# Optimization experiments

Hardware: AMD Instinct MI355X
Metric: run time of the kernel (lower is better)

Reference implementation:

```python
import jax, jax.numpy as jnp
import numpy as np

CROP = 3          # crop_size
MAX_CROP = 2 * CROP  # 6 -> 6x6 = 36 offsets (faithful to range(max_crop))
H = 384


def reference(predict, target, target_mask):
    # mask both images
    t = target * target_mask
    p = predict * target_mask

    B, C, _, _ = p.shape
    hw = H - MAX_CROP  # 378

    # cropped target: [:, :, 3:-3, 3:-3] -> [B, C, 378, 378]
    ct = t[:, :, CROP:-CROP, CROP:-CROP]

    def c_mse_at(u, v):
        # shifted predict window [B, C, 378, 378]
        cp = jax.lax.dynamic_slice(p, (0, 0, u, v), (B, C, hw, hw))
        bb = jnp.mean(ct - cp)           # brightness bias (scalar)
        return jnp.mean((cp + bb - ct) ** 2)  # MSE after bias correction

    offs = jnp.arange(MAX_CROP)
    uu, vv = jnp.meshgrid(offs, offs, indexing='ij')
    losses = jax.vmap(c_mse_at)(uu.ravel(), vv.ravel())  # [36]

    cMSE = jnp.min(losses)
    score = -10.0 * jnp.log10(cMSE)  # cPSNR
    return score


def setup_inputs() -> dict:
    key = jax.random.key(0)
    k1, k2, k3 = jax.random.split(key, 3)
    shape = (32, 1, 384, 384)
    predict = jax.random.uniform(k1, shape, dtype=jnp.float32)
    target = jax.random.uniform(k2, shape, dtype=jnp.float32)
    target_mask = jax.random.uniform(k3, shape, dtype=jnp.float32)
    return {"predict": predict, "target": target, "target_mask": target_mask}
```

## Files before the change

kernel.cpp:

```cpp
#include <hip/hip_runtime.h>
#include <hip/hip_bf16.h>
#include <math.h>


#define NIMG 32
#define IMGSZ (384 * 384)
#define NRT 126
#define NSG 24
#define BSZ 128
#define NCC 756
#define NEDGE 64
#define CCPAD 760
#define CHUNK 95
#define NM 40
#define MSTRIDE 756
#define MQUADS 189
#define NE 262

__global__ __launch_bounds__(BSZ) void probav_fused_kernel(
    const float* __restrict__ predict,
    const float* __restrict__ target,
    const float* __restrict__ mask,
    float* __restrict__ mpart ,
    double* __restrict__ epart ) {

  const int t = threadIdx.x;
  const int lane = t & 63;
  const int w = t >> 6;

  if (blockIdx.x >= NEDGE) {
    const int i = blockIdx.x - NEDGE;
    const int cb = (i & 7) * CHUNK + (i >> 3);
    if (cb >= NCC) return;

    __shared__ float red[2 * NM];

    const int tid = cb * BSZ + t;
    const int img = tid / (NRT * NSG);
    const int rem = tid - img * (NRT * NSG);
    const int rt  = rem / NSG;
    const int sg  = rem - rt * NSG;
    const int r0  = rt * 3;
    const int jb  = sg * 16;
    const size_t base = (size_t)img * IMGSZ;
    const bool isLastRt = (rt == NRT - 1);

    int qc[6];
#pragma unroll
    for (int q = 0; q < 6; ++q) {
      int c = jb + 4 * q;
      qc[q] = (c > 380) ? 380 : c;
    }

    float ct[3][16];
    float t1 = 0.f, t2 = 0.f;
#pragma unroll
    for (int rr = 0; rr < 3; ++rr) {
      const float* trow = target + base + (size_t)(r0 + rr + 3) * 384;
      const float* mrow = mask   + base + (size_t)(r0 + rr + 3) * 384;
      float tv[20], mv[20];
#pragma unroll
      for (int q = 0; q < 5; ++q) {
        float4 a = *reinterpret_cast<const float4*>(trow + qc[q]);
        float4 b = *reinterpret_cast<const float4*>(mrow + qc[q]);
        tv[4 * q + 0] = a.x; tv[4 * q + 1] = a.y; tv[4 * q + 2] = a.z; tv[4 * q + 3] = a.w;
        mv[4 * q + 0] = b.x; mv[4 * q + 1] = b.y; mv[4 * q + 2] = b.z; mv[4 * q + 3] = b.w;
      }
#pragma unroll
      for (int x = 0; x < 16; ++x) {
        float v = tv[3 + x] * mv[3 + x];
        v = (jb + x < 378) ? v : 0.f;
        ct[rr][x] = v;
        t1 += v;
        t2 = fmaf(v, v, t2);
      }
    }

    float cc[36];
#pragma unroll
    for (int o = 0; o < 36; ++o) cc[o] = 0.f;
    float tot1 = 0.f, tot2 = 0.f;
    const int ownR = isLastRt ? 8 : 3;

#pragma unroll
    for (int R = 0; R < 8; ++R) {
      const float* prow = predict + base + (size_t)(r0 + R) * 384;
      const float* mrow = mask    + base + (size_t)(r0 + R) * 384;
      float pm[21];
#pragma unroll
      for (int q = 0; q < 6; ++q) {
        float4 a = *reinterpret_cast<const float4*>(prow + qc[q]);
        float4 b = *reinterpret_cast<const float4*>(mrow + qc[q]);
        if (4 * q + 0 < 21) pm[4 * q + 0] = a.x * b.x;
        if (4 * q + 1 < 21) pm[4 * q + 1] = a.y * b.y;
        if (4 * q + 2 < 21) pm[4 * q + 2] = a.z * b.z;
        if (4 * q + 3 < 21) pm[4 * q + 3] = a.w * b.w;
      }
      if (R < ownR) {
#pragma unroll
        for (int x = 0; x < 16; ++x) {
          tot1 += pm[x];
          tot2 = fmaf(pm[x], pm[x], tot2);
        }
      }
      const int rlo = (R > 5) ? (R - 5) : 0;
      const int rhi = (R < 2) ? R : 2;
#pragma unroll
      for (int rr = rlo; rr <= rhi; ++rr) {
        const int u = R - rr;
#pragma unroll
        for (int v = 0; v < 6; ++v) {
#pragma unroll
          for (int x = 0; x < 16; ++x) {
            cc[u * 6 + v] = fmaf(ct[rr][x], pm[v + x], cc[u * 6 + v]);
          }
        }
      }
    }

#pragma unroll
    for (int o = 0; o < 36; ++o) {
      float a = cc[o];
#pragma unroll
      for (int off = 32; off > 0; off >>= 1) a += __shfl_down(a, off);
      if (lane == 0) red[w * NM + o] = a;
    }
    {
      float a = t1, b = t2, c = tot1, d = tot2;
#pragma unroll
      for (int off = 32; off > 0; off >>= 1) {
        a += __shfl_down(a, off);
        b += __shfl_down(b, off);
        c += __shfl_down(c, off);
        d += __shfl_down(d, off);
      }
      if (lane == 0) { red[w * NM + 36] = a; red[w * NM + 37] = b; red[w * NM + 38] = c; red[w * NM + 39] = d; }
    }
    __syncthreads();
    if (t < NM) {
      mpart[t * MSTRIDE + cb] = red[0 * NM + t] + red[1 * NM + t];
    }
  } else {
    const int img = blockIdx.x >> 1;
    const int slice = blockIdx.x & 1;
    const size_t base = (size_t)img * IMGSZ;

    if (slice == 0) {
      for (int ridx = w; ridx < 10; ridx += 2) {
        const int row = (ridx < 5) ? ridx : (373 + ridx);
        const float* pr = predict + base + (size_t)row * 384;
        const float* mr = mask    + base + (size_t)row * 384;
        double e1 = 0.0, e2 = 0.0;
#pragma unroll
        for (int k = 0; k < 6; ++k) {
          float v = pr[lane + 64 * k] * mr[lane + 64 * k];
          e1 += v;
          e2 += (double)v * v;
        }
#pragma unroll
        for (int off = 32; off > 0; off >>= 1) {
          e1 += __shfl_down(e1, off);
          e2 += __shfl_down(e2, off);
        }
        if (lane == 0) {
          epart[(size_t)ridx        * NIMG + img] = e1;
          epart[(size_t)(10 + ridx) * NIMG + img] = e2;
        }
      }
      if (t < 110) {
        const int ridx = t / 11, cidx = t % 11;
        const int row = (ridx < 5) ? ridx : (373 + ridx);
        const int col = (cidx < 5) ? cidx : (373 + cidx);
        float v = predict[base + (size_t)row * 384 + col] * mask[base + (size_t)row * 384 + col];
        epart[(size_t)(42 + t)  * NIMG + img] = (double)v;
        epart[(size_t)(152 + t) * NIMG + img] = (double)v * v;
      }
    } else {
      for (int cidx = w; cidx < 11; cidx += 2) {
        const int col = (cidx < 5) ? cidx : (373 + cidx);
        double f1 = 0.0, f2 = 0.0;
#pragma unroll
        for (int k = 0; k < 6; ++k) {
          const int r = lane + 64 * k;
          if (r < 383) {
            float v = predict[base + (size_t)r * 384 + col] * mask[base + (size_t)r * 384 + col];
            f1 += v;
            f2 += (double)v * v;
          }
        }
#pragma unroll
        for (int off = 32; off > 0; off >>= 1) {
          f1 += __shfl_down(f1, off);
          f2 += __shfl_down(f2, off);
        }
        if (lane == 0) {
          epart[(size_t)(20 + cidx) * NIMG + img] = f1;
          epart[(size_t)(31 + cidx) * NIMG + img] = f2;
        }
      }
    }
  }
}

__global__ void probav_final_kernel(const float* __restrict__ mpart,
                                    const double* __restrict__ epart,
                                    float* __restrict__ out) {
  __shared__ double M[NM];
  __shared__ double E[NE];
  __shared__ double Etmp[524];
  __shared__ double loss[36];
  const int t = threadIdx.x;
  const int lane = t & 63;
  const int w = t >> 6;

  for (int v = w; v < NM; v += 16) {
    const float4* qp = reinterpret_cast<const float4*>(mpart + v * MSTRIDE);
    double s = 0.0;
    for (int i = lane; i < MQUADS; i += 64) {
      float4 q = qp[i];
      s += (double)q.x + (double)q.y + (double)q.z + (double)q.w;
    }
#pragma unroll
    for (int off = 32; off > 0; off >>= 1) s += __shfl_down(s, off);
    if (lane == 0) M[v] = s;
  }
  if (t < 524) {
    const int e = t >> 1, si = t & 1;
    double s = 0.0;
    for (int i = si * 16; i < si * 16 + 16; ++i) s += epart[(size_t)e * NIMG + i];
    Etmp[t] = s;
  }
  __syncthreads();
  if (t < NE) E[t] = Etmp[2 * t] + Etmp[2 * t + 1];
  __syncthreads();

  if (t < 36) {
    const int u = t / 6, v = t % 6;
    double br1 = 0, br2 = 0, bc1 = 0, bc2 = 0, x1 = 0, x2 = 0;
    int rset[5], nr = 0;
    for (int j = 0; j < u; ++j) rset[nr++] = j;
    for (int j = 5 + u; j < 10; ++j) rset[nr++] = j;
    int cset[6], nc = 0;
    for (int j = 0; j < v; ++j) cset[nc++] = j;
    for (int j = 5 + v; j < 11; ++j) cset[nc++] = j;
    for (int a = 0; a < nr; ++a) { br1 += E[rset[a]]; br2 += E[10 + rset[a]]; }
    for (int b = 0; b < nc; ++b) { bc1 += E[20 + cset[b]]; bc2 += E[31 + cset[b]]; }
    for (int a = 0; a < nr; ++a)
      for (int b = 0; b < nc; ++b) {
        x1 += E[42 + rset[a] * 11 + cset[b]];
        x2 += E[152 + rset[a] * 11 + cset[b]];
      }
    const double T1 = M[36], T2 = M[37];
    const double W1 = M[38] - br1 - bc1 + x1;
    const double W2 = M[39] - br2 - bc2 + x2;
    const double CCv = M[t];
    const double N = 32.0 * 378.0 * 378.0;
    const double S1 = T1 - W1;
    const double S2 = T2 - 2.0 * CCv + W2;
    loss[t] = S2 / N - (S1 / N) * (S1 / N);
  }
  __syncthreads();
  if (t == 0) {
    double best = loss[0];
    for (int o = 1; o < 36; ++o) best = fmin(best, loss[o]);
    out[0] = (float)(-10.0 * log10(best));
  }
}

extern "C" void kernel_launch(void* const* d_in, const int* in_sizes, int n_in,
                              void* d_out, int out_size, void* d_ws, size_t ws_size,
                              hipStream_t stream) {
  const float* predict = (const float*)d_in[0];
  const float* target  = (const float*)d_in[1];
  const float* mask    = (const float*)d_in[2];
  float* out = (float*)d_out;

  float*  mpart = (float*)d_ws;
  double* epart = (double*)((char*)d_ws + NM * MSTRIDE * 4);

  probav_fused_kernel<<<NEDGE + CCPAD, BSZ, 0, stream>>>(predict, target, mask, mpart, epart);
  probav_final_kernel<<<1, 1024, 0, stream>>>(mpart, epart, out);
}
```

Measured before the change: 61.37 us.

## Narrow per-thread column strip to 8 and use 768-thread blocks

```diff
diff --git a/kernel.cpp b/kernel.cpp
--- a/kernel.cpp
+++ b/kernel.cpp
@@ -6,15 +6,15 @@
 #define NIMG 32
 #define IMGSZ (384 * 384)
 #define NRT 126
-#define NSG 24
-#define BSZ 128
-#define NCC 756
+#define NSG 48
+#define BSZ 768
+#define NCC 252
 #define NEDGE 64
-#define CCPAD 760
-#define CHUNK 95
+#define SWZD 256
+#define SCH 32
 #define NM 40
-#define MSTRIDE 756
-#define MQUADS 189
+#define MSTRIDE 252
+#define MQUADS 63
 #define NE 262
 
 __global__ __launch_bounds__(BSZ) void probav_fused_kernel(
@@ -29,11 +29,11 @@
   const int w = t >> 6;
 
   if (blockIdx.x >= NEDGE) {
-    const int i = blockIdx.x - NEDGE;
-    const int cb = (i & 7) * CHUNK + (i >> 3);
+    const int sb = blockIdx.x - NEDGE;
+    const int cb = (sb & 7) * SCH + (sb >> 3);
     if (cb >= NCC) return;
 
-    __shared__ float red[2 * NM];
+    __shared__ float red[12 * NM];
 
     const int tid = cb * BSZ + t;
     const int img = tid / (NRT * NSG);
@@ -41,33 +41,26 @@
     const int rt  = rem / NSG;
     const int sg  = rem - rt * NSG;
     const int r0  = rt * 3;
-    const int jb  = sg * 16;
+    const int jb  = sg * 8;
     const size_t base = (size_t)img * IMGSZ;
     const bool isLastRt = (rt == NRT - 1);
 
-    int qc[6];
-#pragma unroll
-    for (int q = 0; q < 6; ++q) {
-      int c = jb + 4 * q;
-      qc[q] = (c > 380) ? 380 : c;
-    }
-
-    float ct[3][16];
+    float ct[3][8];
     float t1 = 0.f, t2 = 0.f;
 #pragma unroll
     for (int rr = 0; rr < 3; ++rr) {
-      const float* trow = target + base + (size_t)(r0 + rr + 3) * 384;
-      const float* mrow = mask   + base + (size_t)(r0 + rr + 3) * 384;
-      float tv[20], mv[20];
-#pragma unroll
-      for (int q = 0; q < 5; ++q) {
-        float4 a = *reinterpret_cast<const float4*>(trow + qc[q]);
-        float4 b = *reinterpret_cast<const float4*>(mrow + qc[q]);
+      const float4* tq = reinterpret_cast<const float4*>(target + base + (size_t)(r0 + rr + 3) * 384 + jb);
+      const float4* mq = reinterpret_cast<const float4*>(mask   + base + (size_t)(r0 + rr + 3) * 384 + jb);
+      float tv[12], mv[12];
+#pragma unroll
+      for (int q = 0; q < 3; ++q) {
+        float4 a = tq[q];
+        float4 b = mq[q];
         tv[4 * q + 0] = a.x; tv[4 * q + 1] = a.y; tv[4 * q + 2] = a.z; tv[4 * q + 3] = a.w;
         mv[4 * q + 0] = b.x; mv[4 * q + 1] = b.y; mv[4 * q + 2] = b.z; mv[4 * q + 3] = b.w;
       }
 #pragma unroll
-      for (int x = 0; x < 16; ++x) {
+      for (int x = 0; x < 8; ++x) {
         float v = tv[3 + x] * mv[3 + x];
         v = (jb + x < 378) ? v : 0.f;
         ct[rr][x] = v;
@@ -84,21 +77,21 @@
 
 #pragma unroll
     for (int R = 0; R < 8; ++R) {
-      const float* prow = predict + base + (size_t)(r0 + R) * 384;
-      const float* mrow = mask    + base + (size_t)(r0 + R) * 384;
-      float pm[21];
-#pragma unroll
-      for (int q = 0; q < 6; ++q) {
-        float4 a = *reinterpret_cast<const float4*>(prow + qc[q]);
-        float4 b = *reinterpret_cast<const float4*>(mrow + qc[q]);
-        if (4 * q + 0 < 21) pm[4 * q + 0] = a.x * b.x;
-        if (4 * q + 1 < 21) pm[4 * q + 1] = a.y * b.y;
-        if (4 * q + 2 < 21) pm[4 * q + 2] = a.z * b.z;
-        if (4 * q + 3 < 21) pm[4 * q + 3] = a.w * b.w;
+      const float4* pq = reinterpret_cast<const float4*>(predict + base + (size_t)(r0 + R) * 384 + jb);
+      const float4* mq = reinterpret_cast<const float4*>(mask    + base + (size_t)(r0 + R) * 384 + jb);
+      float pm[16];
+#pragma unroll
+      for (int q = 0; q < 4; ++q) {
+        float4 a = pq[q];
+        float4 b = mq[q];
+        pm[4 * q + 0] = a.x * b.x;
+        pm[4 * q + 1] = a.y * b.y;
+        pm[4 * q + 2] = a.z * b.z;
+        pm[4 * q + 3] = a.w * b.w;
       }
       if (R < ownR) {
 #pragma unroll
-        for (int x = 0; x < 16; ++x) {
+        for (int x = 0; x < 8; ++x) {
           tot1 += pm[x];
           tot2 = fmaf(pm[x], pm[x], tot2);
         }
@@ -111,7 +104,7 @@
 #pragma unroll
         for (int v = 0; v < 6; ++v) {
 #pragma unroll
-          for (int x = 0; x < 16; ++x) {
+          for (int x = 0; x < 8; ++x) {
             cc[u * 6 + v] = fmaf(ct[rr][x], pm[v + x], cc[u * 6 + v]);
           }
         }
@@ -138,7 +131,10 @@
     }
     __syncthreads();
     if (t < NM) {
-      mpart[t * MSTRIDE + cb] = red[0 * NM + t] + red[1 * NM + t];
+      float v = 0.f;
+#pragma unroll
+      for (int k = 0; k < 12; ++k) v += red[k * NM + t];
+      mpart[t * MSTRIDE + cb] = v;
     }
   } else {
     const int img = blockIdx.x >> 1;
@@ -146,7 +142,8 @@
     const size_t base = (size_t)img * IMGSZ;
 
     if (slice == 0) {
-      for (int ridx = w; ridx < 10; ridx += 2) {
+      if (w < 10) {
+        const int ridx = w;
         const int row = (ridx < 5) ? ridx : (373 + ridx);
         const float* pr = predict + base + (size_t)row * 384;
         const float* mr = mask    + base + (size_t)row * 384;
@@ -167,16 +164,18 @@
           epart[(size_t)(10 + ridx) * NIMG + img] = e2;
         }
       }
-      if (t < 110) {
-        const int ridx = t / 11, cidx = t % 11;
+      if (t >= 640 && t < 750) {
+        const int k = t - 640;
+        const int ridx = k / 11, cidx = k % 11;
         const int row = (ridx < 5) ? ridx : (373 + ridx);
         const int col = (cidx < 5) ? cidx : (373 + cidx);
         float v = predict[base + (size_t)row * 384 + col] * mask[base + (size_t)row * 384 + col];
-        epart[(size_t)(42 + t)  * NIMG + img] = (double)v;
-        epart[(size_t)(152 + t) * NIMG + img] = (double)v * v;
+        epart[(size_t)(42 + k)  * NIMG + img] = (double)v;
+        epart[(size_t)(152 + k) * NIMG + img] = (double)v * v;
       }
     } else {
-      for (int cidx = w; cidx < 11; cidx += 2) {
+      if (w < 11) {
+        const int cidx = w;
         const int col = (cidx < 5) ? cidx : (373 + cidx);
         double f1 = 0.0, f2 = 0.0;
 #pragma unroll
@@ -278,6 +277,6 @@
   float*  mpart = (float*)d_ws;
   double* epart = (double*)((char*)d_ws + NM * MSTRIDE * 4);
 
-  probav_fused_kernel<<<NEDGE + CCPAD, BSZ, 0, stream>>>(predict, target, mask, mpart, epart);
+  probav_fused_kernel<<<NEDGE + SWZD, BSZ, 0, stream>>>(predict, target, mask, mpart, epart);
   probav_final_kernel<<<1, 1024, 0, stream>>>(mpart, epart, out);
 }
```

New measurement: 60.87 us. Within noise of the previous version (-0.8%).
